# Kernel optimization log

Hardware: AMD Instinct MI355X
Metric: run time of the kernel (lower is better)

## Reference

```python
import jax, jax.numpy as jnp
import numpy as np

ALPHA, GAMMA = 0.25, 2.0
W_CLS, W_REG, W_DIR = 1.0, 2.0, 0.2
X_MIN, X_MAX = 0.0, 200.0
Y_MIN, Y_MAX = -50.0, 50.0
SX = 0.2 * 2  # voxel_size_x * backbone_stride
SY = 0.2 * 2
IGNORE_R = 1
CLS_CH = 0  # anchor_id*num_classes + car_class_id


def _bce_logits(x, t):
    # numerically stable BCE-with-logits, matches F.binary_cross_entropy_with_logits
    return jnp.maximum(x, 0.0) - x * t + jnp.log1p(jnp.exp(-jnp.abs(x)))


def _build_targets(gt_boxes, B, H, W):
    # gt_boxes: [B, N, 8] = (x, y, z, l, w, h, rot, cls_id)
    x, y, z, l, w_, h, rot, cid = [gt_boxes[..., i] for i in range(8)]
    valid = (cid == 0.0) & (x >= X_MIN) & (x < X_MAX) & (y >= Y_MIN) & (y < Y_MAX)
    gx = jnp.floor((x - X_MIN) / SX).astype(jnp.int32)
    gy = jnp.floor((y - Y_MIN) / SY).astype(jnp.int32)
    valid &= (gx >= 0) & (gx < W) & (gy >= 0) & (gy < H)

    bidx = jnp.broadcast_to(jnp.arange(B)[:, None], x.shape)
    BHW = B * H * W
    flat = (bidx * H + gy) * W + gx                      # [B, N]
    flat = jnp.where(valid, flat, BHW).reshape(-1)        # sentinel -> dropped scatter

    cls_t = jnp.zeros((BHW,), jnp.float32).at[flat].set(1.0, mode='drop')

    cell_cx = X_MIN + (gx.astype(jnp.float32) + 0.5) * SX
    cell_cy = Y_MIN + (gy.astype(jnp.float32) + 0.5) * SY
    dx = (x - cell_cx) / SX
    dy = (y - cell_cy) / SY
    vals = jnp.stack([dx, dy, z,
                      jnp.log(jnp.maximum(l, 1e-3)),
                      jnp.log(jnp.maximum(w_, 1e-3)),
                      jnp.log(jnp.maximum(h, 1e-3)),
                      jnp.sin(rot)], axis=0).reshape(7, -1)   # [7, B*N]
    reg_t = jnp.zeros((7, BHW), jnp.float32).at[:, flat].set(vals, mode='drop')

    dir_bin = jnp.where(jnp.cos(rot) >= 0.0, 0, 1).reshape(-1)
    dir_t = jnp.zeros((2, BHW), jnp.float32).at[dir_bin, flat].set(1.0, mode='drop')

    pos = jnp.zeros((BHW,), bool).at[flat].set(True, mode='drop')  # reg_mask == dir_mask

    # ignore-radius window around each positive on the car cls channel
    ign = jnp.zeros((BHW,), bool)
    gxf, gyf, bf, vf = gx.reshape(-1), gy.reshape(-1), bidx.reshape(-1), valid.reshape(-1)
    for oy in range(-IGNORE_R, IGNORE_R + 1):
        for ox in range(-IGNORE_R, IGNORE_R + 1):
            gy2, gx2 = gyf + oy, gxf + ox
            ok = vf & (gy2 >= 0) & (gy2 < H) & (gx2 >= 0) & (gx2 < W)
            f2 = jnp.where(ok, (bf * H + gy2) * W + gx2, BHW)
            ign = ign.at[f2].set(True, mode='drop')
    cls_valid_ch = (~ign) | pos  # box centers always stay valid

    return (cls_t.reshape(B, H, W), reg_t.reshape(7, B, H, W),
            dir_t.reshape(2, B, H, W), cls_valid_ch.reshape(B, H, W),
            pos.reshape(B, H, W))


def reference(cls_pred, reg_pred, dir_pred, gt_boxes, batch_size):
    B, _, H, W = cls_pred.shape
    cls_t1, reg_t, dir_t, cls_valid1, pos = _build_targets(gt_boxes, B, H, W)

    cls_target = jnp.zeros_like(cls_pred).at[:, CLS_CH].set(cls_t1)
    cls_valid = jnp.ones(cls_pred.shape, bool).at[:, CLS_CH].set(cls_valid1)
    reg_target = jnp.moveaxis(reg_t, 1, 0)  # [B, 7, H, W]
    dir_target = jnp.moveaxis(dir_t, 1, 0)  # [B, 2, H, W]

    # focal loss, masked
    p = jax.nn.sigmoid(cls_pred)
    bce = _bce_logits(cls_pred, cls_target)
    p_t = p * cls_target + (1.0 - p) * (1.0 - cls_target)
    a_t = ALPHA * cls_target + (1.0 - ALPHA) * (1.0 - cls_target)
    vm = cls_valid.astype(cls_pred.dtype)
    cls_loss = jnp.sum(a_t * (1.0 - p_t) ** GAMMA * bce * vm) / jnp.maximum(vm.sum(), 1.0)

    # smooth L1 on positive cells (mean over 7*npos masked elements)
    posf = pos[:, None].astype(reg_pred.dtype)  # [B, 1, H, W]
    d = jnp.abs(reg_pred - reg_target)
    sl1 = jnp.where(d < 1.0, 0.5 * d * d, d - 0.5)
    n_reg = posf.sum() * 7.0
    reg_loss = jnp.sum(sl1 * posf) / jnp.maximum(n_reg, 1.0)

    # direction BCE on positive cells (mean over 2*npos masked elements)
    dbce = _bce_logits(dir_pred, dir_target)
    n_dir = posf.sum() * 2.0
    dir_loss = jnp.sum(dbce * posf) / jnp.maximum(n_dir, 1.0)

    total = W_CLS * cls_loss + W_REG * reg_loss + W_DIR * dir_loss
    return total, cls_loss, reg_loss, dir_loss


def setup_inputs() -> dict:
    key = jax.random.key(0)
    ks = jax.random.split(key, 11)
    B, H, W, N = 16, 250, 500, 64
    cls_pred = jax.random.normal(ks[0], (B, 3, H, W), jnp.float32)
    reg_pred = jax.random.normal(ks[1], (B, 7, H, W), jnp.float32)
    dir_pred = jax.random.normal(ks[2], (B, 2, H, W), jnp.float32)
    x = jax.random.uniform(ks[3], (B, N)) * 210.0 - 5.0
    y = jax.random.uniform(ks[4], (B, N)) * 110.0 - 55.0
    z = jax.random.uniform(ks[5], (B, N)) * 3.0 - 1.5
    l = jax.random.uniform(ks[6], (B, N)) * 2.0 + 3.0
    w = jax.random.uniform(ks[7], (B, N)) * 0.7 + 1.5
    h = jax.random.uniform(ks[8], (B, N)) * 0.8 + 1.2
    rot = jax.random.uniform(ks[9], (B, N)) * (2.0 * np.pi) - np.pi
    cid = jax.random.randint(ks[10], (B, N), 0, 3).astype(jnp.float32)
    gt_boxes = jnp.stack([x, y, z, l, w, h, rot, cid], axis=-1)
    return {"cls_pred": cls_pred, "reg_pred": reg_pred, "dir_pred": dir_pred,
            "gt_boxes": gt_boxes, "batch_size": B}
```

## Files before the change

### kernel.cpp

```cpp
#include <hip/hip_runtime.h>


#define B_   16
#define NC_  3
#define H_   250
#define W_   500
#define N_   64
#define HW_  125000
#define TOTAL_CLS 6000000
#define N4   1500000
#define PLANE_WORDS 3907
#define TBLB 128
#define DGRID 1024
#define THREADS 256

#define PART_OFF 8
#define NPART (DGRID + B_)

__device__ __forceinline__ void sig_bce0(float x, float& p, float& bce0) {
    float ax = fabsf(x);
    float em = __expf(-ax);
    float lg = __logf(1.0f + em);
    bce0 = fmaxf(x, 0.0f) + lg;
    float r1 = __fdividef(1.0f, 1.0f + em);
    p = (x >= 0.0f) ? r1 : em * r1;
}

__device__ __forceinline__ float focal0(float x) {
    float p, bce0; sig_bce0(x, p, bce0);
    return 0.75f * p * p * bce0;
}

__device__ __forceinline__ float focal_delta(float x) {
    float p, bce0; sig_bce0(x, p, bce0);
    float q = 1.0f - p;
    return 0.25f * q * q * (bce0 - x) - 0.75f * p * p * bce0;
}

__global__ __launch_bounds__(THREADS) void dense_kernel(
        const float* __restrict__ cls, float* __restrict__ ws_f) {
    const float4* c4 = (const float4*)cls;
    float sum = 0.0f;
    const int stride = DGRID * THREADS;
    for (int k = blockIdx.x * THREADS + threadIdx.x; k < N4; k += stride) {
        float4 v = c4[k];
        sum += focal0(v.x) + focal0(v.y) + focal0(v.z) + focal0(v.w);
    }
    #pragma unroll
    for (int off = 32; off > 0; off >>= 1) sum += __shfl_down(sum, off, 64);
    __shared__ float sw[4];
    int lane = threadIdx.x & 63, wv = threadIdx.x >> 6;
    if (lane == 0) sw[wv] = sum;
    __syncthreads();
    if (threadIdx.x == 0)
        ws_f[PART_OFF + blockIdx.x] = sw[0] + sw[1] + sw[2] + sw[3];
}

__global__ __launch_bounds__(THREADS) void box_kernel(
        const float* __restrict__ cls, const float* __restrict__ reg,
        const float* __restrict__ dirp, const float* __restrict__ gt,
        unsigned* __restrict__ ws) {
    __shared__ unsigned s_pos[PLANE_WORDS];
    __shared__ unsigned s_ign[PLANE_WORDS];
    __shared__ unsigned s_keys[TBLB], s_maxv[TBLB], s_bins[TBLB];
    __shared__ float    s_f[3];
    __shared__ unsigned s_u[2];
    const int tid = threadIdx.x;
    const int b = blockIdx.x;

    for (int i = tid; i < PLANE_WORDS; i += THREADS) { s_pos[i] = 0u; s_ign[i] = 0u; }
    for (int i = tid; i < TBLB; i += THREADS) {
        s_keys[i] = 0xFFFFFFFFu; s_maxv[i] = 0u; s_bins[i] = 0u;
    }
    if (tid < 3) s_f[tid] = 0.0f;
    if (tid < 2) s_u[tid] = 0u;
    __syncthreads();

    bool valid = false;
    int gx = 0, gy = 0, pix = 0, slot = -1;
    float x = 0, y = 0, z = 0, l = 0, wb = 0, h = 0, rot = 0;
    if (tid < N_) {
        const float4* g4 = (const float4*)(gt + (b * N_ + tid) * 8);
        float4 p0 = g4[0], p1 = g4[1];
        x = p0.x; y = p0.y; z = p0.z; l = p0.w;
        wb = p1.x; h = p1.y; rot = p1.z;
        float cid = p1.w;
        valid = (cid == 0.0f) && (x >= 0.0f) && (x < 200.0f) &&
                (y >= -50.0f) && (y < 50.0f);
        if (valid) {
            gx = (int)floorf(x / 0.4f);
            gy = (int)floorf((y + 50.0f) / 0.4f);
            valid = (gx >= 0) && (gx < W_) && (gy >= 0) && (gy < H_);
        }
        if (valid) {
            pix = gy * W_ + gx;
            atomicOr(&s_pos[pix >> 5], 1u << (pix & 31));
            for (int oy = -1; oy <= 1; ++oy) {
                int gy2 = gy + oy;
                if (gy2 < 0 || gy2 >= H_) continue;
                for (int ox = -1; ox <= 1; ++ox) {
                    int gx2 = gx + ox;
                    if (gx2 < 0 || gx2 >= W_) continue;
                    int f2 = gy2 * W_ + gx2;
                    atomicOr(&s_ign[f2 >> 5], 1u << (f2 & 31));
                }
            }
            unsigned bin = (cosf(rot) >= 0.0f) ? 0u : 1u;
            unsigned hsh = ((unsigned)pix * 2654435761u) >> 25;
            for (;;) {
                unsigned old = atomicCAS(&s_keys[hsh], 0xFFFFFFFFu, (unsigned)pix);
                if (old == 0xFFFFFFFFu || old == (unsigned)pix) break;
                hsh = (hsh + 1u) & (TBLB - 1u);
            }
            slot = (int)hsh;
            atomicMax(&s_maxv[slot], (unsigned)(tid + 1));
            atomicOr(&s_bins[slot], 1u << bin);
        }
    }
    __syncthreads();

    if (valid && s_maxv[slot] == (unsigned)(tid + 1)) {
        float cx = ((float)gx + 0.5f) * 0.4f;
        float cy = -50.0f + ((float)gy + 0.5f) * 0.4f;
        float tgt[7] = {(x - cx) / 0.4f, (y - cy) / 0.4f, z,
                        logf(fmaxf(l, 1e-3f)), logf(fmaxf(wb, 1e-3f)),
                        logf(fmaxf(h, 1e-3f)), sinf(rot)};
        float my_reg = 0.0f;
        #pragma unroll
        for (int c = 0; c < 7; ++c) {
            float d = fabsf(reg[(b * 7 + c) * HW_ + pix] - tgt[c]);
            my_reg += (d < 1.0f) ? 0.5f * d * d : d - 0.5f;
        }
        unsigned u = s_bins[slot];
        float my_dir = 0.0f;
        #pragma unroll
        for (int c = 0; c < 2; ++c) {
            float xd = dirp[(b * 2 + c) * HW_ + pix];
            float t = (float)((u >> c) & 1u);
            float ax = fabsf(xd);
            my_dir += fmaxf(xd, 0.0f) - xd * t + __logf(1.0f + __expf(-ax));
        }
        atomicAdd(&s_f[1], my_reg);
        atomicAdd(&s_f[2], my_dir);
        atomicAdd(&s_u[1], 1u);
    }

    const float* cls0 = cls + (b * NC_) * HW_;
    float corr = 0.0f;
    unsigned cign = 0u;
    for (int wd = tid; wd < PLANE_WORDS; wd += THREADS) {
        unsigned iw = s_ign[wd], pw = s_pos[wd];
        unsigned m1 = iw & ~pw;
        while (m1) {
            int bit = __ffs(m1) - 1; m1 &= m1 - 1;
            corr -= focal0(cls0[(wd << 5) + bit]);
            cign++;
        }
        unsigned m2 = pw;
        while (m2) {
            int bit = __ffs(m2) - 1; m2 &= m2 - 1;
            corr += focal_delta(cls0[(wd << 5) + bit]);
        }
    }
    if (corr != 0.0f) atomicAdd(&s_f[0], corr);
    if (cign) atomicAdd(&s_u[0], cign);
    __syncthreads();

    if (tid == 0) {
        float* fws = (float*)ws;
        fws[PART_OFF + DGRID + b] = s_f[0];
        atomicAdd(&fws[0], s_f[1]);
        atomicAdd(&fws[1], s_f[2]);
        atomicAdd(&ws[2], s_u[0]);
        atomicAdd(&ws[3], s_u[1]);
    }
}

__global__ __launch_bounds__(THREADS) void fin_kernel(
        const unsigned* __restrict__ ws, float* __restrict__ out) {
    const float* fws = (const float*)ws;
    float s = 0.0f;
    for (int k = threadIdx.x; k < NPART; k += THREADS)
        s += fws[PART_OFF + k];
    #pragma unroll
    for (int off = 32; off > 0; off >>= 1) s += __shfl_down(s, off, 64);
    __shared__ float sw[4];
    int lane = threadIdx.x & 63, wv = threadIdx.x >> 6;
    if (lane == 0) sw[wv] = s;
    __syncthreads();
    if (threadIdx.x == 0) {
        float cs = sw[0] + sw[1] + sw[2] + sw[3];
        float rs = fws[0], ds = fws[1];
        float ic = (float)ws[2], np = (float)ws[3];
        float vm = (float)TOTAL_CLS - ic;
        float cls_loss = cs / fmaxf(vm, 1.0f);
        float reg_loss = rs / fmaxf(np * 7.0f, 1.0f);
        float dir_loss = ds / fmaxf(np * 2.0f, 1.0f);
        out[0] = cls_loss + 2.0f * reg_loss + 0.2f * dir_loss;
        out[1] = cls_loss;
        out[2] = reg_loss;
        out[3] = dir_loss;
    }
}

extern "C" void kernel_launch(void* const* d_in, const int* in_sizes, int n_in,
                              void* d_out, int out_size, void* d_ws, size_t ws_size,
                              hipStream_t stream) {
    const float* cls_pred = (const float*)d_in[0];
    const float* reg_pred = (const float*)d_in[1];
    const float* dir_pred = (const float*)d_in[2];
    const float* gt_boxes = (const float*)d_in[3];
    unsigned* ws = (unsigned*)d_ws;
    float* out = (float*)d_out;

    hipMemsetAsync(ws, 0, 16, stream);
    box_kernel<<<B_, THREADS, 0, stream>>>(cls_pred, reg_pred, dir_pred, gt_boxes, ws);
    dense_kernel<<<DGRID, THREADS, 0, stream>>>(cls_pred, (float*)ws);
    fin_kernel<<<1, THREADS, 0, stream>>>(ws, out);
}
```

Measured before the change: 133.7 us.

## Fuse box and dense kernels, replace bitplanes with hashed sparse ignore list

Merges the per-batch box kernel and the dense focal-loss kernel into one launch, with the first 16 blocks doing box work and the rest doing the dense sweep. It drops the memset by writing per-batch partials instead of using global atomics. The box path stops clearing and scanning a full bitplane of the spatial grid and instead collects ignore cells into a shared hash set and list, resolving duplicate boxes with wave shuffles. This removes launch overhead and the per-block scan over 3907 words, but makes the box blocks more complex.

```diff
diff --git a/kernel.cpp b/kernel.cpp
--- a/kernel.cpp
+++ b/kernel.cpp
@@ -9,13 +9,14 @@
 #define HW_  125000
 #define TOTAL_CLS 6000000
 #define N4   1500000
-#define PLANE_WORDS 3907
-#define TBLB 128
-#define DGRID 1024
 #define THREADS 256
-
-#define PART_OFF 8
-#define NPART (DGRID + B_)
+#define DENSE_BLOCKS 1024
+#define GRID (B_ + DENSE_BLOCKS)
+
+#define HSLOTS 1024
+#define ILIST  576
+
+#define CLS_OFF 64
 
 __device__ __forceinline__ void sig_bce0(float x, float& p, float& bce0) {
     float ax = fabsf(x);
@@ -25,175 +26,188 @@
     float r1 = __fdividef(1.0f, 1.0f + em);
     p = (x >= 0.0f) ? r1 : em * r1;
 }
-
 __device__ __forceinline__ float focal0(float x) {
-    float p, bce0; sig_bce0(x, p, bce0);
-    return 0.75f * p * p * bce0;
-}
-
+    float p, b; sig_bce0(x, p, b);
+    return 0.75f * p * p * b;
+}
 __device__ __forceinline__ float focal_delta(float x) {
-    float p, bce0; sig_bce0(x, p, bce0);
+    float p, b; sig_bce0(x, p, b);
     float q = 1.0f - p;
-    return 0.25f * q * q * (bce0 - x) - 0.75f * p * p * bce0;
-}
-
-__global__ __launch_bounds__(THREADS) void dense_kernel(
-        const float* __restrict__ cls, float* __restrict__ ws_f) {
-    const float4* c4 = (const float4*)cls;
-    float sum = 0.0f;
-    const int stride = DGRID * THREADS;
-    for (int k = blockIdx.x * THREADS + threadIdx.x; k < N4; k += stride) {
-        float4 v = c4[k];
-        sum += focal0(v.x) + focal0(v.y) + focal0(v.z) + focal0(v.w);
-    }
-    #pragma unroll
-    for (int off = 32; off > 0; off >>= 1) sum += __shfl_down(sum, off, 64);
-    __shared__ float sw[4];
-    int lane = threadIdx.x & 63, wv = threadIdx.x >> 6;
-    if (lane == 0) sw[wv] = sum;
-    __syncthreads();
-    if (threadIdx.x == 0)
-        ws_f[PART_OFF + blockIdx.x] = sw[0] + sw[1] + sw[2] + sw[3];
-}
-
-__global__ __launch_bounds__(THREADS) void box_kernel(
+    return 0.25f * q * q * (b - x) - 0.75f * p * p * b;
+}
+
+__global__ __launch_bounds__(THREADS) void main_kernel(
         const float* __restrict__ cls, const float* __restrict__ reg,
         const float* __restrict__ dirp, const float* __restrict__ gt,
-        unsigned* __restrict__ ws) {
-    __shared__ unsigned s_pos[PLANE_WORDS];
-    __shared__ unsigned s_ign[PLANE_WORDS];
-    __shared__ unsigned s_keys[TBLB], s_maxv[TBLB], s_bins[TBLB];
-    __shared__ float    s_f[3];
-    __shared__ unsigned s_u[2];
+        float* __restrict__ fws) {
+    __shared__ unsigned s_hash[HSLOTS];
+    __shared__ unsigned s_list[ILIST];
+    __shared__ unsigned s_pospix[N_];
+    __shared__ unsigned s_cnt[2];
+    __shared__ float    s_acc[3];
+    __shared__ unsigned s_uacc;
+    __shared__ float    sw[4];
     const int tid = threadIdx.x;
+
+    if (blockIdx.x >= B_) {
+        const int gbid = blockIdx.x - B_;
+        const float4* c4 = (const float4*)cls;
+        float s0 = 0.f, s1 = 0.f, s2 = 0.f, s3 = 0.f;
+        const int stride = DENSE_BLOCKS * THREADS;
+        for (int k = gbid * THREADS + tid; k < N4; k += stride) {
+            float4 v = c4[k];
+            s0 += focal0(v.x); s1 += focal0(v.y);
+            s2 += focal0(v.z); s3 += focal0(v.w);
+        }
+        float sum = (s0 + s1) + (s2 + s3);
+        #pragma unroll
+        for (int off = 32; off > 0; off >>= 1) sum += __shfl_down(sum, off, 64);
+        if ((tid & 63) == 0) sw[tid >> 6] = sum;
+        __syncthreads();
+        if (tid == 0) fws[CLS_OFF + blockIdx.x] = (sw[0] + sw[1]) + (sw[2] + sw[3]);
+        return;
+    }
+
     const int b = blockIdx.x;
-
-    for (int i = tid; i < PLANE_WORDS; i += THREADS) { s_pos[i] = 0u; s_ign[i] = 0u; }
-    for (int i = tid; i < TBLB; i += THREADS) {
-        s_keys[i] = 0xFFFFFFFFu; s_maxv[i] = 0u; s_bins[i] = 0u;
-    }
-    if (tid < 3) s_f[tid] = 0.0f;
-    if (tid < 2) s_u[tid] = 0u;
-    __syncthreads();
-
-    bool valid = false;
-    int gx = 0, gy = 0, pix = 0, slot = -1;
-    float x = 0, y = 0, z = 0, l = 0, wb = 0, h = 0, rot = 0;
-    if (tid < N_) {
+    for (int i = tid; i < HSLOTS; i += THREADS) s_hash[i] = 0xFFFFFFFFu;
+    if (tid < 2) s_cnt[tid] = 0u;
+    if (tid < 3) s_acc[tid] = 0.f;
+    if (tid == 0) s_uacc = 0u;
+    __syncthreads();
+
+    float my_reg = 0.f, my_dir = 0.f, my_corr = 0.f;
+    unsigned my_cign = 0u;
+
+    if (tid < 64) {
         const float4* g4 = (const float4*)(gt + (b * N_ + tid) * 8);
         float4 p0 = g4[0], p1 = g4[1];
-        x = p0.x; y = p0.y; z = p0.z; l = p0.w;
-        wb = p1.x; h = p1.y; rot = p1.z;
-        float cid = p1.w;
-        valid = (cid == 0.0f) && (x >= 0.0f) && (x < 200.0f) &&
-                (y >= -50.0f) && (y < 50.0f);
+        float x = p0.x, y = p0.y, z = p0.z, l = p0.w;
+        float wb = p1.x, h = p1.y, rot = p1.z, cid = p1.w;
+        bool valid = (cid == 0.0f) && (x >= 0.0f) && (x < 200.0f) &&
+                     (y >= -50.0f) && (y < 50.0f);
+        int gx = 0, gy = 0;
         if (valid) {
             gx = (int)floorf(x / 0.4f);
             gy = (int)floorf((y + 50.0f) / 0.4f);
             valid = (gx >= 0) && (gx < W_) && (gy >= 0) && (gy < H_);
         }
+        const int pix = gy * W_ + gx;
+        const unsigned bin = (cosf(rot) >= 0.0f) ? 1u : 2u;
+
+        unsigned long long vm = __ballot(valid);
+        int last = -1; unsigned ub = 0u;
+        for (int l2 = 0; l2 < 64; ++l2) {
+            int p2 = __shfl(pix, l2, 64);
+            unsigned b2 = __shfl(bin, l2, 64);
+            if (valid && ((vm >> l2) & 1ull) && p2 == pix) { last = l2; ub |= b2; }
+        }
+        bool winner = valid && (last == tid);
+        if (winner) s_pospix[atomicAdd(&s_cnt[1], 1u)] = (unsigned)pix;
+
         if (valid) {
-            pix = gy * W_ + gx;
-            atomicOr(&s_pos[pix >> 5], 1u << (pix & 31));
             for (int oy = -1; oy <= 1; ++oy) {
-                int gy2 = gy + oy;
-                if (gy2 < 0 || gy2 >= H_) continue;
+                int gy2 = gy + oy; if (gy2 < 0 || gy2 >= H_) continue;
                 for (int ox = -1; ox <= 1; ++ox) {
-                    int gx2 = gx + ox;
-                    if (gx2 < 0 || gx2 >= W_) continue;
-                    int f2 = gy2 * W_ + gx2;
-                    atomicOr(&s_ign[f2 >> 5], 1u << (f2 & 31));
+                    int gx2 = gx + ox; if (gx2 < 0 || gx2 >= W_) continue;
+                    unsigned cell = (unsigned)(gy2 * W_ + gx2);
+                    unsigned hh = (cell * 2654435761u) >> 22;
+                    for (;;) {
+                        unsigned old = atomicCAS(&s_hash[hh], 0xFFFFFFFFu, cell);
+                        if (old == 0xFFFFFFFFu) {
+                            s_list[atomicAdd(&s_cnt[0], 1u)] = cell;
+                            break;
+                        }
+                        if (old == cell) break;
+                        hh = (hh + 1u) & (HSLOTS - 1u);
+                    }
                 }
             }
-            unsigned bin = (cosf(rot) >= 0.0f) ? 0u : 1u;
-            unsigned hsh = ((unsigned)pix * 2654435761u) >> 25;
-            for (;;) {
-                unsigned old = atomicCAS(&s_keys[hsh], 0xFFFFFFFFu, (unsigned)pix);
-                if (old == 0xFFFFFFFFu || old == (unsigned)pix) break;
-                hsh = (hsh + 1u) & (TBLB - 1u);
+        }
+
+        if (winner) {
+            float cx = ((float)gx + 0.5f) * 0.4f;
+            float cy = -50.0f + ((float)gy + 0.5f) * 0.4f;
+            float tgt[7] = {(x - cx) / 0.4f, (y - cy) / 0.4f, z,
+                            logf(fmaxf(l, 1e-3f)), logf(fmaxf(wb, 1e-3f)),
+                            logf(fmaxf(h, 1e-3f)), sinf(rot)};
+            #pragma unroll
+            for (int c = 0; c < 7; ++c) {
+                float d = fabsf(reg[(b * 7 + c) * HW_ + pix] - tgt[c]);
+                my_reg += (d < 1.0f) ? 0.5f * d * d : d - 0.5f;
             }
-            slot = (int)hsh;
-            atomicMax(&s_maxv[slot], (unsigned)(tid + 1));
-            atomicOr(&s_bins[slot], 1u << bin);
-        }
-    }
-    __syncthreads();
-
-    if (valid && s_maxv[slot] == (unsigned)(tid + 1)) {
-        float cx = ((float)gx + 0.5f) * 0.4f;
-        float cy = -50.0f + ((float)gy + 0.5f) * 0.4f;
-        float tgt[7] = {(x - cx) / 0.4f, (y - cy) / 0.4f, z,
-                        logf(fmaxf(l, 1e-3f)), logf(fmaxf(wb, 1e-3f)),
-                        logf(fmaxf(h, 1e-3f)), sinf(rot)};
-        float my_reg = 0.0f;
-        #pragma unroll
-        for (int c = 0; c < 7; ++c) {
-            float d = fabsf(reg[(b * 7 + c) * HW_ + pix] - tgt[c]);
-            my_reg += (d < 1.0f) ? 0.5f * d * d : d - 0.5f;
-        }
-        unsigned u = s_bins[slot];
-        float my_dir = 0.0f;
-        #pragma unroll
-        for (int c = 0; c < 2; ++c) {
-            float xd = dirp[(b * 2 + c) * HW_ + pix];
-            float t = (float)((u >> c) & 1u);
-            float ax = fabsf(xd);
-            my_dir += fmaxf(xd, 0.0f) - xd * t + __logf(1.0f + __expf(-ax));
-        }
-        atomicAdd(&s_f[1], my_reg);
-        atomicAdd(&s_f[2], my_dir);
-        atomicAdd(&s_u[1], 1u);
-    }
-
-    const float* cls0 = cls + (b * NC_) * HW_;
-    float corr = 0.0f;
-    unsigned cign = 0u;
-    for (int wd = tid; wd < PLANE_WORDS; wd += THREADS) {
-        unsigned iw = s_ign[wd], pw = s_pos[wd];
-        unsigned m1 = iw & ~pw;
-        while (m1) {
-            int bit = __ffs(m1) - 1; m1 &= m1 - 1;
-            corr -= focal0(cls0[(wd << 5) + bit]);
-            cign++;
-        }
-        unsigned m2 = pw;
-        while (m2) {
-            int bit = __ffs(m2) - 1; m2 &= m2 - 1;
-            corr += focal_delta(cls0[(wd << 5) + bit]);
-        }
-    }
-    if (corr != 0.0f) atomicAdd(&s_f[0], corr);
-    if (cign) atomicAdd(&s_u[0], cign);
-    __syncthreads();
-
+            #pragma unroll
+            for (int c = 0; c < 2; ++c) {
+                float xd = dirp[(b * 2 + c) * HW_ + pix];
+                float t = (float)((ub >> c) & 1u);
+                my_dir += fmaxf(xd, 0.0f) - xd * t + __logf(1.0f + __expf(-fabsf(xd)));
+            }
+            my_corr += focal_delta(cls[(b * NC_) * HW_ + pix]);
+        }
+    }
+    __syncthreads();
+
+    {
+        const float* cls0 = cls + (b * NC_) * HW_;
+        const unsigned icnt = s_cnt[0], pcnt = s_cnt[1];
+        for (unsigned i = tid; i < icnt; i += THREADS) {
+            unsigned cell = s_list[i];
+            bool isp = false;
+            for (unsigned j = 0; j < pcnt; ++j) isp |= (s_pospix[j] == cell);
+            if (!isp) { my_corr -= focal0(cls0[cell]); my_cign++; }
+        }
+    }
+
+    #pragma unroll
+    for (int off = 32; off > 0; off >>= 1) {
+        my_corr += __shfl_down(my_corr, off, 64);
+        my_reg  += __shfl_down(my_reg,  off, 64);
+        my_dir  += __shfl_down(my_dir,  off, 64);
+        my_cign += __shfl_down(my_cign, off, 64);
+    }
+    if ((tid & 63) == 0) {
+        atomicAdd(&s_acc[0], my_corr);
+        atomicAdd(&s_acc[1], my_reg);
+        atomicAdd(&s_acc[2], my_dir);
+        atomicAdd(&s_uacc, my_cign);
+    }
+    __syncthreads();
     if (tid == 0) {
-        float* fws = (float*)ws;
-        fws[PART_OFF + DGRID + b] = s_f[0];
-        atomicAdd(&fws[0], s_f[1]);
-        atomicAdd(&fws[1], s_f[2]);
-        atomicAdd(&ws[2], s_u[0]);
-        atomicAdd(&ws[3], s_u[1]);
+        fws[b]        = s_acc[1];
+        fws[16 + b]   = s_acc[2];
+        ((unsigned*)fws)[32 + b] = s_uacc;
+        ((unsigned*)fws)[48 + b] = s_cnt[1];
+        fws[CLS_OFF + b] = s_acc[0];
     }
 }
 
 __global__ __launch_bounds__(THREADS) void fin_kernel(
-        const unsigned* __restrict__ ws, float* __restrict__ out) {
-    const float* fws = (const float*)ws;
-    float s = 0.0f;
-    for (int k = threadIdx.x; k < NPART; k += THREADS)
-        s += fws[PART_OFF + k];
+        const float* __restrict__ fws, float* __restrict__ out) {
+    const unsigned* uws = (const unsigned*)fws;
+    float cs = 0.f;
+    for (int k = threadIdx.x; k < GRID; k += THREADS) cs += fws[CLS_OFF + k];
+    float rs = 0.f, ds = 0.f, ic = 0.f, np = 0.f;
+    if (threadIdx.x < B_) {
+        rs = fws[threadIdx.x];
+        ds = fws[16 + threadIdx.x];
+        ic = (float)uws[32 + threadIdx.x];
+        np = (float)uws[48 + threadIdx.x];
+    }
     #pragma unroll
-    for (int off = 32; off > 0; off >>= 1) s += __shfl_down(s, off, 64);
+    for (int off = 32; off > 0; off >>= 1) {
+        cs += __shfl_down(cs, off, 64);
+        rs += __shfl_down(rs, off, 64);
+        ds += __shfl_down(ds, off, 64);
+        ic += __shfl_down(ic, off, 64);
+        np += __shfl_down(np, off, 64);
+    }
     __shared__ float sw[4];
     int lane = threadIdx.x & 63, wv = threadIdx.x >> 6;
-    if (lane == 0) sw[wv] = s;
+    if (lane == 0) sw[wv] = cs;
     __syncthreads();
     if (threadIdx.x == 0) {
-        float cs = sw[0] + sw[1] + sw[2] + sw[3];
-        float rs = fws[0], ds = fws[1];
-        float ic = (float)ws[2], np = (float)ws[3];
+        float cst = (sw[0] + sw[1]) + (sw[2] + sw[3]);
         float vm = (float)TOTAL_CLS - ic;
-        float cls_loss = cs / fmaxf(vm, 1.0f);
+        float cls_loss = cst / fmaxf(vm, 1.0f);
         float reg_loss = rs / fmaxf(np * 7.0f, 1.0f);
         float dir_loss = ds / fmaxf(np * 2.0f, 1.0f);
         out[0] = cls_loss + 2.0f * reg_loss + 0.2f * dir_loss;
@@ -210,11 +224,10 @@
     const float* reg_pred = (const float*)d_in[1];
     const float* dir_pred = (const float*)d_in[2];
     const float* gt_boxes = (const float*)d_in[3];
-    unsigned* ws = (unsigned*)d_ws;
+    float* fws = (float*)d_ws;
     float* out = (float*)d_out;
 
-    hipMemsetAsync(ws, 0, 16, stream);
-    box_kernel<<<B_, THREADS, 0, stream>>>(cls_pred, reg_pred, dir_pred, gt_boxes, ws);
-    dense_kernel<<<DGRID, THREADS, 0, stream>>>(cls_pred, (float*)ws);
-    fin_kernel<<<1, THREADS, 0, stream>>>(ws, out);
-}
+    main_kernel<<<GRID, THREADS, 0, stream>>>(cls_pred, reg_pred, dir_pred,
+                                              gt_boxes, fws);
+    fin_kernel<<<1, THREADS, 0, stream>>>(fws, out);
+}
```

After: 117.4 us. 12.2% less time.
